# Kernel tuning notes

Hardware: AMD Instinct MI355X
Metric: run time of the kernel (lower is better)

The kernel has to match this reference:

```python
import jax, jax.numpy as jnp
import numpy as np

B, V, C, H, W, D = 1, 3, 32, 320, 320, 32


def setup_inputs() -> dict:
    key = jax.random.key(0)
    ks = jax.random.split(key, 14)
    feats = jax.random.normal(ks[0], (B, V, C, H, W), jnp.float32)
    # Valid pinhole projections: P = [[K @ [R|t]], [0,0,0,1]], identity rotation,
    # horizontal baselines sized so the warp stays mostly in-image over the depth range.
    K = np.array([[400.0, 0.0, W / 2.0], [0.0, 400.0, H / 2.0], [0.0, 0.0, 1.0]])
    mats = []
    for tx in (0.0, 100.0, -100.0):
        Rt = np.eye(4)
        Rt[0, 3] = tx
        P = np.eye(4)
        P[:3, :4] = K @ Rt[:3, :4]
        mats.append(P)
    proj = jnp.asarray(np.broadcast_to(np.stack(mats)[None], (B, V, 4, 4)).copy(), jnp.float32)
    planes = jnp.linspace(425.0, 935.0, D, dtype=jnp.float32)
    depth_values = jnp.broadcast_to(planes[None, :, None, None], (B, D, H, W)).astype(jnp.float32)
    s = 0.05  # small init so exp(reg_cost) stays well-scaled
    W0 = s * jax.random.normal(ks[1], (8, C, 3, 3), jnp.float32)
    Ws1 = s * jax.random.normal(ks[2], (8, 8, 3, 3), jnp.float32)
    W1 = s * jax.random.normal(ks[3], (16, 8, 3, 3), jnp.float32)
    Ws2 = s * jax.random.normal(ks[4], (16, 16, 3, 3), jnp.float32)
    W2 = s * jax.random.normal(ks[5], (32, 16, 3, 3), jnp.float32)
    Ws3 = s * jax.random.normal(ks[6], (32, 32, 3, 3), jnp.float32)
    W3 = s * jax.random.normal(ks[7], (64, 32, 3, 3), jnp.float32)
    Ws4 = s * jax.random.normal(ks[8], (64, 64, 3, 3), jnp.float32)
    U4 = s * jax.random.normal(ks[9], (32, 64, 1, 1), jnp.float32)
    U3 = s * jax.random.normal(ks[10], (16, 32, 1, 1), jnp.float32)
    U2 = s * jax.random.normal(ks[11], (8, 16, 1, 1), jnp.float32)
    Wout = s * jax.random.normal(ks[12], (1, 8, 3, 3), jnp.float32)
    return dict(feats=feats, proj=proj, depth_values=depth_values, W0=W0, Ws1=Ws1,
                W1=W1, Ws2=Ws2, W2=W2, Ws3=Ws3, W3=W3, Ws4=Ws4, U4=U4, U3=U3, U2=U2, Wout=Wout)


def _conv(x, w, stride=1):
    return jax.lax.conv_general_dilated(x, w, (stride, stride), 'SAME',
                                        dimension_numbers=('NCHW', 'OIHW', 'NCHW'))


def _up2(x):
    return jnp.repeat(jnp.repeat(x, 2, axis=2), 2, axis=3)


def _bilinear(img, x, y):
    # img [C,H,W]; x,y [N] pixel coords; zero padding, align_corners semantics
    Cc, Hh, Ww = img.shape
    x0 = jnp.floor(x)
    y0 = jnp.floor(y)
    wx = x - x0
    wy = y - y0

    def tap(xi, yi):
        valid = ((xi >= 0) & (xi <= Ww - 1) & (yi >= 0) & (yi <= Hh - 1)).astype(img.dtype)
        xc = jnp.clip(xi, 0, Ww - 1).astype(jnp.int32)
        yc = jnp.clip(yi, 0, Hh - 1).astype(jnp.int32)
        return img[:, yc, xc] * valid  # [C,N]

    return (tap(x0, y0) * (1 - wx) * (1 - wy) + tap(x0 + 1, y0) * wx * (1 - wy)
            + tap(x0, y0 + 1) * (1 - wx) * wy + tap(x0 + 1, y0 + 1) * wx * wy)


def _forward(feats, proj, depth_values, W0, Ws1, W1, Ws2, W2, Ws3, W3, Ws4, U4, U3, U2, Wout):
    Bn, Vn, Cn, Hn, Wn = feats.shape
    Dn = depth_values.shape[1]
    N = Hn * Wn
    relu = jax.nn.relu
    ref = feats[:, 0]
    ref_sq = ref * ref
    # Precompute per-src-view rotated pixel rays and translations.
    inv_ref = jnp.linalg.inv(proj[:, 0])                       # [B,4,4]
    rel = jnp.einsum('bvij,bjk->bvik', proj[:, 1:], inv_ref)   # [B,V-1,4,4]
    rot, trans = rel[:, :, :3, :3], rel[:, :, :3, 3]
    ys, xs = jnp.meshgrid(jnp.arange(Hn), jnp.arange(Wn), indexing='ij')
    pix = jnp.stack([xs.ravel(), ys.ravel(), jnp.ones(N)], 0).astype(feats.dtype)  # [3,N]
    rot_pix = jnp.einsum('bvij,jn->bvin', rot, pix)            # [B,V-1,3,N]

    def regularize(x, s1, s2, s3, s4):
        c1 = relu(_conv(x, W0) + _conv(s1, Ws1))
        c2 = relu(_conv(c1, W1, 2) + _conv(s2, Ws2))
        c3 = relu(_conv(c2, W2, 2) + _conv(s3, Ws3))
        c4 = relu(_conv(c3, W3, 2) + _conv(s4, Ws4))
        u3 = c3 + _up2(_conv(c4, U4))
        u2 = c2 + _up2(_conv(u3, U3))
        u1 = c1 + _up2(_conv(u2, U2))
        return _conv(u1, Wout), c1, c2, c3, c4

    def step(carry, depth_slice):  # depth_slice [B,H,W]
        s1, s2, s3, s4, exp_sum, depth_img, max_prob = carry
        vol_sum, vol_sq = ref, ref_sq
        dflat = depth_slice.reshape(Bn, 1, N)
        for v in range(Vn - 1):
            xyz = rot_pix[:, v] * dflat + trans[:, v, :, None]   # [B,3,N]
            px = xyz[:, 0] / xyz[:, 2]
            py = xyz[:, 1] / xyz[:, 2]
            warped = jax.vmap(_bilinear)(feats[:, v + 1], px, py).reshape(Bn, Cn, Hn, Wn)
            vol_sum = vol_sum + warped
            vol_sq = vol_sq + warped * warped
        variance = vol_sq / Vn - (vol_sum / Vn) ** 2
        cost, s1, s2, s3, s4 = regularize(variance, s1, s2, s3, s4)
        prob = jnp.exp(cost)                                     # [B,1,H,W]
        max_prob = jnp.maximum(max_prob, prob)                   # == flag*prob + (1-flag)*max
        depth_img = depth_img + depth_slice[:, None] * prob
        exp_sum = exp_sum + prob
        return (s1, s2, s3, s4, exp_sum, depth_img, max_prob), None

    z = lambda c, h, w: jnp.zeros((Bn, c, h, w), feats.dtype)
    init = (z(8, Hn, Wn), z(16, Hn // 2, Wn // 2), z(32, Hn // 4, Wn // 4), z(64, Hn // 8, Wn // 8),
            z(1, Hn, Wn), z(1, Hn, Wn), z(1, Hn, Wn))
    carry, _ = jax.lax.scan(step, init, jnp.moveaxis(depth_values, 1, 0))
    _, _, _, _, exp_sum, depth_img, max_prob = carry
    es = exp_sum + 1e-10
    depth_map = (depth_img / es)[:, 0]
    prob_map = (max_prob / es)[:, 0]
    return jnp.stack([depth_map, prob_map], axis=1)  # [B,2,H,W]


def reference(feats, proj, depth_values, W0, Ws1, W1, Ws2, W2, Ws3, W3, Ws4, U4, U3, U2, Wout):
    return _forward(feats, proj, depth_values, W0, Ws1, W1, Ws2, W2, Ws3, W3, Ws4, U4, U3, U2, Wout)
```

## Files before the change

kernel.cpp:

```cpp
#include <hip/hip_runtime.h>
#include <hip/hip_fp16.h>
#include <math.h>

#define HH 320
#define WW 320
#define NP (HH*WW)
#define CC 32
#define DD 32

#define H2 160
#define W2 160
#define N2 (H2*W2)
#define H4 80
#define W4 80
#define N4 (H4*W4)
#define H8 40
#define W8 40
#define N8 (H8*W8)

#define HALO 18
#define NHALO (HALO*HALO)

#define C1SZ (8*NP)
#define C2SZ (16*N2)
#define C3SZ (32*N4)
#define C4SZ (64*N8)

#define SMEM_FLOATS 5344

#define OFF_REL   0
#define OFF_C1R   64
#define OFF_C2R   (OFF_C1R + 5*C1SZ)
#define OFF_C3R   (OFF_C2R + 4*C2SZ)
#define OFF_C4R   (OFF_C3R + 3*C3SZ)
#define OFF_ESUM  (OFF_C4R + 2*C4SZ)
#define OFF_DIMG  (OFF_ESUM + NP)
#define OFF_MAXP  (OFF_DIMG + NP)
#define OFF_ACCE  (OFF_MAXP + NP)
#define OFF_FT    OFF_ACCE
#define OFF_END   (OFF_FT + (3*CC*NP)/2)

__global__ void k_prep(const float* __restrict__ proj, float* __restrict__ rel) {
    if (threadIdx.x != 0 || blockIdx.x != 0) return;
    float a[4][4], inv[4][4];
#pragma unroll
    for (int i = 0; i < 4; i++)
#pragma unroll
        for (int j = 0; j < 4; j++) {
            a[i][j] = proj[i*4 + j];
            inv[i][j] = (i == j) ? 1.0f : 0.0f;
        }
#pragma unroll
    for (int c = 0; c < 4; c++) {
        float s = 1.0f / a[c][c];
#pragma unroll
        for (int j = 0; j < 4; j++) { a[c][j] *= s; inv[c][j] *= s; }
#pragma unroll
        for (int r = 0; r < 4; r++) if (r != c) {
            float f = a[r][c];
#pragma unroll
            for (int j = 0; j < 4; j++) {
                a[r][j] -= f * a[c][j];
                inv[r][j] -= f * inv[c][j];
            }
        }
    }
#pragma unroll
    for (int v = 1; v < 3; v++) {
        const float* P = proj + v*16;
        float rm[3][4];
#pragma unroll
        for (int i = 0; i < 3; i++)
#pragma unroll
            for (int j = 0; j < 4; j++) {
                float s = 0.0f;
#pragma unroll
                for (int k = 0; k < 4; k++) s += P[i*4 + k] * inv[k][j];
                rm[i][j] = s;
            }
        float* o = rel + (v-1)*12;
        o[0]=rm[0][0]; o[1]=rm[0][1]; o[2]=rm[0][2];
        o[3]=rm[1][0]; o[4]=rm[1][1]; o[5]=rm[1][2];
        o[6]=rm[2][0]; o[7]=rm[2][1]; o[8]=rm[2][2];
        o[9]=rm[0][3]; o[10]=rm[1][3]; o[11]=rm[2][3];
    }
}

__global__ __launch_bounds__(256) void k_transpose(const float* __restrict__ feats,
                                                   __half* __restrict__ featsT) {
    __shared__ float lds[32][65];
    int g = blockIdx.x;
    int v = g / 1600;
    int p0 = (g - v*1600) * 64;
    const float* src = feats + (size_t)v*CC*NP + p0;
    for (int i = threadIdx.x; i < 32*64; i += 256) {
        int c = i >> 6, pp = i & 63;
        lds[c][pp] = src[(size_t)c*NP + pp];
    }
    __syncthreads();
    __half* dst = featsT + ((size_t)v*NP + p0)*32;
    int pp = threadIdx.x >> 2, cq = (threadIdx.x & 3) * 8;
    __half2 h[4];
#pragma unroll
    for (int j = 0; j < 4; j++)
        h[j] = __floats2half2_rn(lds[cq+2*j][pp], lds[cq+2*j+1][pp]);
    *(float4*)(dst + (size_t)pp*32 + cq) = *(float4*)h;
}

__device__ __forceinline__ void set_hline16(const __half* base, float* s) {
    const float4* q = (const float4*)base;
#pragma unroll
    for (int i = 0; i < 2; i++) {
        float4 raw = q[i];
        const __half2* h2 = (const __half2*)&raw;
#pragma unroll
        for (int j = 0; j < 4; j++) {
            float2 f = __half22float2(h2[j]);
            s[i*8 + 2*j]     = f.x;
            s[i*8 + 2*j + 1] = f.y;
        }
    }
}
__device__ __forceinline__ void acc_hline16(const __half* base, float w, float* t) {
    const float4* q = (const float4*)base;
#pragma unroll
    for (int i = 0; i < 2; i++) {
        float4 raw = q[i];
        const __half2* h2 = (const __half2*)&raw;
#pragma unroll
        for (int j = 0; j < 4; j++) {
            float2 f = __half22float2(h2[j]);
            t[i*8 + 2*j]     += f.x * w;
            t[i*8 + 2*j + 1] += f.y * w;
        }
    }
}

__device__ __forceinline__ int band_tile(int blk) { return (blk & 7) * 50 + (blk >> 3); }


__device__ void stageA(int blk, int d, int useT,
        const float* __restrict__ feats, const __half* __restrict__ featsT,
        const float* __restrict__ rel,
        const float* __restrict__ depthv, const float* __restrict__ c1r,
        const float* __restrict__ W0, const float* __restrict__ Ws1,
        float* smem) {
    __half2* pbuf = (__half2*)smem;
    float* fbuf = smem;
    const float* dslice = depthv + (size_t)d * NP;
    const float* s1 = c1r + (size_t)((d+4)%5) * C1SZ;
    float* c1out = (float*)c1r + (size_t)(d%5) * C1SZ;

    int L = band_tile(blk);
    int bx = L % 20, by = L / 20;
    int ox0 = bx*16, oy0 = by*16;

    const float inv3 = 1.0f / 3.0f;

    int opx = threadIdx.x & 15, opy = threadIdx.x >> 4;
    int obase = opy*HALO + opx;
    int outp = (oy0 + opy)*WW + ox0 + opx;

#pragma unroll 1
    for (int s = 0; s < 2; s++) {
        int hp = threadIdx.x + s*256;
        if (hp >= NHALO) break;
        int hy = hp / HALO, hx = hp - hy*HALO;
        int gy = oy0 + hy - 1, gx = ox0 + hx - 1;
        if (gy < 0 || gy >= HH || gx < 0 || gx >= WW) {
            __half2 z = __floats2half2_rn(0.0f, 0.0f);
#pragma unroll 1
            for (int c = 0; c < 16; c++) pbuf[c*NHALO + hp] = z;
            continue;
        }
        int p = gy*WW + gx;
        float depth = dslice[p];
        float fx = (float)gx, fy = (float)gy;

        int offs[8]; float wts[8];
#pragma unroll 1
        for (int v = 0; v < 2; v++) {
            const float* r = rel + v*12;
            float X = (r[0]*fx + r[1]*fy + r[2]) * depth + r[9];
            float Y = (r[3]*fx + r[4]*fy + r[5]) * depth + r[10];
            float Z = (r[6]*fx + r[7]*fy + r[8]) * depth + r[11];
            float iz = 1.0f / Z;
            float px = X * iz, py = Y * iz;
            float x0f = floorf(px), y0f = floorf(py);
            float wx = px - x0f, wy = py - y0f;
            int x0 = (int)x0f, y0 = (int)y0f;
#pragma unroll
            for (int t = 0; t < 4; t++) {
                int xi = x0 + (t & 1), yi = y0 + (t >> 1);
                float wgt = ((t & 1) ? wx : 1.0f - wx) * ((t >> 1) ? wy : 1.0f - wy);
                bool valid = (xi >= 0) && (xi <= WW-1) && (yi >= 0) && (yi <= HH-1);
                int xc = min(max(xi, 0), WW-1);
                int yc = min(max(yi, 0), HH-1);
                offs[v*4 + t] = yc*WW + xc;
                wts[v*4 + t] = valid ? wgt : 0.0f;
            }
        }

#pragma unroll 1
        for (int half = 0; half < 2; half++) {
            int cb = half * 16;
            float sum[16], sq[16], t[16];
            if (useT) {
                set_hline16(featsT + ((size_t)p << 5) + cb, sum);
#pragma unroll
                for (int c = 0; c < 16; c++) sq[c] = sum[c]*sum[c];
#pragma unroll 1
                for (int v = 0; v < 2; v++) {
                    const __half* fv = featsT + (size_t)(v+1)*CC*NP;
#pragma unroll
                    for (int c = 0; c < 16; c++) t[c] = 0.0f;
#pragma unroll 1
                    for (int tp = 0; tp < 4; tp++)
                        acc_hline16(fv + ((size_t)offs[v*4+tp] << 5) + cb,
                                    wts[v*4+tp], t);
#pragma unroll
                    for (int c = 0; c < 16; c++) { sum[c] += t[c]; sq[c] += t[c]*t[c]; }
                }
            } else {
                const float* f1 = feats + CC*NP;
                const float* f2 = feats + 2*CC*NP;
#pragma unroll 1
                for (int c = 0; c < 16; c++) {
                    int cg = cb + c;
                    float rv = feats[cg*NP + p];
                    const float* b1 = f1 + cg*NP;
                    float t1 = b1[offs[0]]*wts[0] + b1[offs[1]]*wts[1]
                             + b1[offs[2]]*wts[2] + b1[offs[3]]*wts[3];
                    const float* b2 = f2 + cg*NP;
                    float t2 = b2[offs[4]]*wts[4] + b2[offs[5]]*wts[5]
                             + b2[offs[6]]*wts[6] + b2[offs[7]]*wts[7];
                    sum[c] = rv + t1 + t2;
                    sq[c]  = rv*rv + t1*t1 + t2*t2;
                }
            }
#pragma unroll
            for (int c = 0; c < 8; c++) {
                float m0 = sum[2*c] * inv3,   v0 = sq[2*c] * inv3 - m0*m0;
                float m1 = sum[2*c+1] * inv3, v1 = sq[2*c+1] * inv3 - m1*m1;
                pbuf[(half*8 + c)*NHALO + hp] = __floats2half2_rn(v0, v1);
            }
        }
    }
    __syncthreads();

    float acc[8];
#pragma unroll
    for (int o = 0; o < 8; o++) acc[o] = 0.0f;

#pragma unroll 1
    for (int cp = 0; cp < 16; cp++) {
        float t0[9], t1[9];
#pragma unroll
        for (int ky = 0; ky < 3; ky++)
#pragma unroll
            for (int kx = 0; kx < 3; kx++) {
                __half2 h = pbuf[cp*NHALO + obase + ky*HALO + kx];
                t0[ky*3+kx] = __low2float(h);
                t1[ky*3+kx] = __high2float(h);
            }
#pragma unroll
        for (int o = 0; o < 8; o++) {
            const float* w0 = W0 + (o*32 + 2*cp)*9;
            float a = acc[o];
#pragma unroll
            for (int k = 0; k < 9; k++) a += t0[k] * w0[k];
#pragma unroll
            for (int k = 0; k < 9; k++) a += t1[k] * w0[9 + k];
            acc[o] = a;
        }
    }
    __syncthreads();

#pragma unroll 1
    for (int hp = threadIdx.x; hp < NHALO; hp += 256) {
        int hy = hp / HALO, hx = hp - hy*HALO;
        int gy = oy0 + hy - 1, gx = ox0 + hx - 1;
        bool v = (gy >= 0) && (gy < HH) && (gx >= 0) && (gx < WW);
        int p = v ? gy*WW + gx : 0;
#pragma unroll
        for (int c = 0; c < 8; c++) fbuf[c*NHALO + hp] = v ? s1[c*NP + p] : 0.0f;
    }
    __syncthreads();
#pragma unroll 1
    for (int ci = 0; ci < 8; ci++) {
        float t[9];
#pragma unroll
        for (int ky = 0; ky < 3; ky++)
#pragma unroll
            for (int kx = 0; kx < 3; kx++) t[ky*3+kx] = fbuf[ci*NHALO + obase + ky*HALO + kx];
#pragma unroll
        for (int o = 0; o < 8; o++) {
            const float* w = Ws1 + (o*8 + ci)*9;
            float a = acc[o];
#pragma unroll
            for (int k = 0; k < 9; k++) a += t[k] * w[k];
            acc[o] = a;
        }
    }
#pragma unroll
    for (int o = 0; o < 8; o++) c1out[o*NP + outp] = fmaxf(acc[o], 0.0f);
}

__device__ void stageB(int blk, int d,
        const float* __restrict__ c1r, const float* __restrict__ c2r_,
        const float* __restrict__ W1, const float* __restrict__ Ws2) {
    const float* c1 = c1r + (size_t)(d%5) * C1SZ;
    const float* s2 = c2r_ + (size_t)((d+3)%4) * C2SZ;
    float* c2 = (float*)c2r_ + (size_t)(d%4) * C2SZ;
    int p = (blk % 100)*256 + threadIdx.x;
    if (p >= N2) return;
    int og = blk / 100;
    int y = p / W2, x = p - y*W2;
    int offsA[9]; float mskA[9];
#pragma unroll
    for (int k = 0; k < 9; k++) {
        int yy = 2*y + k/3, xx = 2*x + k%3;
        bool v = (yy < HH) && (xx < WW);
        offsA[k] = v ? yy*WW + xx : 0;
        mskA[k] = v ? 1.0f : 0.0f;
    }
    int offsB[9]; float mskB[9];
#pragma unroll
    for (int k = 0; k < 9; k++) {
        int yy = y + k/3 - 1, xx = x + k%3 - 1;
        bool v = (yy >= 0) && (yy < H2) && (xx >= 0) && (xx < W2);
        offsB[k] = v ? yy*W2 + xx : 0;
        mskB[k] = v ? 1.0f : 0.0f;
    }
    float acc[8];
#pragma unroll
    for (int o = 0; o < 8; o++) acc[o] = 0.0f;
#pragma unroll 1
    for (int ci = 0; ci < 8; ci++) {
        const float* b = c1 + ci*NP;
        float t[9];
#pragma unroll
        for (int k = 0; k < 9; k++) t[k] = b[offsA[k]] * mskA[k];
#pragma unroll
        for (int o = 0; o < 8; o++) {
            const float* w = W1 + ((og*8 + o)*8 + ci)*9;
            float a = acc[o];
#pragma unroll
            for (int k = 0; k < 9; k++) a += t[k] * w[k];
            acc[o] = a;
        }
    }
#pragma unroll 1
    for (int ci = 0; ci < 16; ci++) {
        const float* b = s2 + ci*N2;
        float t[9];
#pragma unroll
        for (int k = 0; k < 9; k++) t[k] = b[offsB[k]] * mskB[k];
#pragma unroll
        for (int o = 0; o < 8; o++) {
            const float* w = Ws2 + ((og*8 + o)*16 + ci)*9;
            float a = acc[o];
#pragma unroll
            for (int k = 0; k < 9; k++) a += t[k] * w[k];
            acc[o] = a;
        }
    }
#pragma unroll
    for (int o = 0; o < 8; o++) c2[(og*8 + o)*N2 + p] = fmaxf(acc[o], 0.0f);
}

__device__ void stageC(int blk, int d,
        const float* __restrict__ c2r_, const float* __restrict__ c3r_,
        const float* __restrict__ W2w, const float* __restrict__ Ws3) {
    const float* c2 = c2r_ + (size_t)(d%4) * C2SZ;
    const float* s3 = c3r_ + (size_t)((d+2)%3) * C3SZ;
    float* c3 = (float*)c3r_ + (size_t)(d%3) * C3SZ;
    int p = (blk % 25)*256 + threadIdx.x;
    if (p >= N4) return;
    int og = blk / 25;
    int y = p / W4, x = p - y*W4;
    int offsA[9]; float mskA[9];
#pragma unroll
    for (int k = 0; k < 9; k++) {
        int yy = 2*y + k/3, xx = 2*x + k%3;
        bool v = (yy < H2) && (xx < W2);
        offsA[k] = v ? yy*W2 + xx : 0;
        mskA[k] = v ? 1.0f : 0.0f;
    }
    int offsB[9]; float mskB[9];
#pragma unroll
    for (int k = 0; k < 9; k++) {
        int yy = y + k/3 - 1, xx = x + k%3 - 1;
        bool v = (yy >= 0) && (yy < H4) && (xx >= 0) && (xx < W4);
        offsB[k] = v ? yy*W4 + xx : 0;
        mskB[k] = v ? 1.0f : 0.0f;
    }
    float acc[8];
#pragma unroll
    for (int o = 0; o < 8; o++) acc[o] = 0.0f;
#pragma unroll 1
    for (int ci = 0; ci < 16; ci++) {
        const float* b = c2 + ci*N2;
        float t[9];
#pragma unroll
        for (int k = 0; k < 9; k++) t[k] = b[offsA[k]] * mskA[k];
#pragma unroll
        for (int o = 0; o < 8; o++) {
            const float* w = W2w + ((og*8 + o)*16 + ci)*9;
            float a = acc[o];
#pragma unroll
            for (int k = 0; k < 9; k++) a += t[k] * w[k];
            acc[o] = a;
        }
    }
#pragma unroll 1
    for (int ci = 0; ci < 32; ci++) {
        const float* b = s3 + ci*N4;
        float t[9];
#pragma unroll
        for (int k = 0; k < 9; k++) t[k] = b[offsB[k]] * mskB[k];
#pragma unroll
        for (int o = 0; o < 8; o++) {
            const float* w = Ws3 + ((og*8 + o)*32 + ci)*9;
            float a = acc[o];
#pragma unroll
            for (int k = 0; k < 9; k++) a += t[k] * w[k];
            acc[o] = a;
        }
    }
#pragma unroll
    for (int o = 0; o < 8; o++) c3[(og*8 + o)*N4 + p] = fmaxf(acc[o], 0.0f);
}

__device__ void stageD(int blk, int d,
        const float* __restrict__ c3r_, const float* __restrict__ c4r_,
        const float* __restrict__ W3w, const float* __restrict__ Ws4) {
    const float* c3 = c3r_ + (size_t)(d%3) * C3SZ;
    const float* s4 = c4r_ + (size_t)((d+1)%2) * C4SZ;
    float* c4 = (float*)c4r_ + (size_t)(d%2) * C4SZ;
    int p = (blk % 7)*256 + threadIdx.x;
    if (p >= N8) return;
    int og = blk / 7;
    int y = p / W8, x = p - y*W8;
    int offsA[9]; float mskA[9];
#pragma unroll
    for (int k = 0; k < 9; k++) {
        int yy = 2*y + k/3, xx = 2*x + k%3;
        bool v = (yy < H4) && (xx < W4);
        offsA[k] = v ? yy*W4 + xx : 0;
        mskA[k] = v ? 1.0f : 0.0f;
    }
    int offsB[9]; float mskB[9];
#pragma unroll
    for (int k = 0; k < 9; k++) {
        int yy = y + k/3 - 1, xx = x + k%3 - 1;
        bool v = (yy >= 0) && (yy < H8) && (xx >= 0) && (xx < W8);
        offsB[k] = v ? yy*W8 + xx : 0;
        mskB[k] = v ? 1.0f : 0.0f;
    }
    float acc[8];
#pragma unroll
    for (int o = 0; o < 8; o++) acc[o] = 0.0f;
#pragma unroll 1
    for (int ci = 0; ci < 32; ci++) {
        const float* b = c3 + ci*N4;
        float t[9];
#pragma unroll
        for (int k = 0; k < 9; k++) t[k] = b[offsA[k]] * mskA[k];
#pragma unroll
        for (int o = 0; o < 8; o++) {
            const float* w = W3w + ((og*8 + o)*32 + ci)*9;
            float a = acc[o];
#pragma unroll
            for (int k = 0; k < 9; k++) a += t[k] * w[k];
            acc[o] = a;
        }
    }
#pragma unroll 1
    for (int ci = 0; ci < 64; ci++) {
        const float* b = s4 + ci*N8;
        float t[9];
#pragma unroll
        for (int k = 0; k < 9; k++) t[k] = b[offsB[k]] * mskB[k];
#pragma unroll
        for (int o = 0; o < 8; o++) {
            const float* w = Ws4 + ((og*8 + o)*64 + ci)*9;
            float a = acc[o];
#pragma unroll
            for (int k = 0; k < 9; k++) a += t[k] * w[k];
            acc[o] = a;
        }
    }
#pragma unroll
    for (int o = 0; o < 8; o++) c4[(og*8 + o)*N8 + p] = fmaxf(acc[o], 0.0f);
}

__device__ void stageU(int blk, int d,
        const float* __restrict__ c1r, const float* __restrict__ c2r_,
        const float* __restrict__ c3r_, const float* __restrict__ c4r_,
        const float* __restrict__ U4, const float* __restrict__ U3,
        const float* __restrict__ U2, const float* __restrict__ Wout,
        const float* __restrict__ depthv,
        float* __restrict__ exp_sum, float* __restrict__ depth_img,
        float* __restrict__ max_prob, float* smem) {
    const float* c1 = c1r + (size_t)(d%5) * C1SZ;
    const float* c2 = c2r_ + (size_t)(d%4) * C2SZ;
    const float* c3 = c3r_ + (size_t)(d%3) * C3SZ;
    const float* c4 = c4r_ + (size_t)(d%2) * C4SZ;
    const float* dslice = depthv + (size_t)d * NP;
    float* u3s = smem;
    float* u2s = smem + 32*36;
    float* u1s = smem + 32*36 + 16*100;

    int L = band_tile(blk);
    int bx = L % 20, by = L / 20;
    int ox0 = bx*16, oy0 = by*16;
    int qy0 = (oy0 >> 2) - 1, qx0 = (ox0 >> 2) - 1;
    int hy0 = (oy0 >> 1) - 1, hx0 = (ox0 >> 1) - 1;

#pragma unroll 1
    for (int i = threadIdx.x; i < 32*36; i += 256) {
        int ch = i / 36, pp = i - ch*36;
        int y4 = qy0 + pp/6, x4 = qx0 + pp%6;
        int y4c = min(max(y4, 0), H4-1), x4c = min(max(x4, 0), W4-1);
        int pl = (y4c >> 1)*W8 + (x4c >> 1);
        const float* w = U4 + ch*64;
        float s = c3[ch*N4 + y4c*W4 + x4c];
#pragma unroll 8
        for (int ci = 0; ci < 64; ci++) s += c4[ci*N8 + pl] * w[ci];
        u3s[ch*36 + pp] = s;
    }
    __syncthreads();
#pragma unroll 1
    for (int i = threadIdx.x; i < 16*100; i += 256) {
        int ch = i / 100, pp = i - ch*100;
        int y2 = hy0 + pp/10, x2 = hx0 + pp%10;
        int y2c = min(max(y2, 0), H2-1), x2c = min(max(x2, 0), W2-1);
        int ly = (y2c >> 1) - qy0, lx = (x2c >> 1) - qx0;
        const float* w = U3 + ch*32;
        float s = c2[ch*N2 + y2c*W2 + x2c];
#pragma unroll 8
        for (int ci = 0; ci < 32; ci++) s += u3s[ci*36 + ly*6 + lx] * w[ci];
        u2s[ch*100 + pp] = s;
    }
    __syncthreads();
#pragma unroll 1
    for (int i = threadIdx.x; i < 8*NHALO; i += 256) {
        int ch = i / NHALO, pp = i - ch*NHALO;
        int gy = oy0 + pp/HALO - 1, gx = ox0 + pp%HALO - 1;
        float s = 0.0f;
        if (gy >= 0 && gy < HH && gx >= 0 && gx < WW) {
            int ly = (gy >> 1) - hy0, lx = (gx >> 1) - hx0;
            const float* w = U2 + ch*16;
            s = c1[ch*NP + gy*WW + gx];
#pragma unroll
            for (int ci = 0; ci < 16; ci++) s += u2s[ci*100 + ly*10 + lx] * w[ci];
        }
        u1s[ch*NHALO + pp] = s;
    }
    __syncthreads();
    int px = threadIdx.x & 15, py = threadIdx.x >> 4;
    int base = py*HALO + px;
    float cost = 0.0f;
#pragma unroll 1
    for (int ci = 0; ci < 8; ci++) {
        const float* w = Wout + ci*9;
#pragma unroll
        for (int ky = 0; ky < 3; ky++)
#pragma unroll
            for (int kx = 0; kx < 3; kx++)
                cost += u1s[ci*NHALO + base + ky*HALO + kx] * w[ky*3 + kx];
    }
    int p = (oy0 + py)*WW + ox0 + px;
    float prob = expf(cost);
    exp_sum[p] += prob;
    depth_img[p] += dslice[p] * prob;
    max_prob[p] = fmaxf(max_prob[p], prob);
}

__global__ __launch_bounds__(256, 5) void k_uber(
        int t, int useT,
        const float* __restrict__ feats, const __half* __restrict__ featsT,
        const float* __restrict__ rel,
        const float* __restrict__ depthv,
        const float* __restrict__ W0, const float* __restrict__ Ws1,
        const float* __restrict__ W1, const float* __restrict__ Ws2,
        const float* __restrict__ W2w, const float* __restrict__ Ws3,
        const float* __restrict__ W3w, const float* __restrict__ Ws4,
        const float* __restrict__ U4, const float* __restrict__ U3,
        const float* __restrict__ U2, const float* __restrict__ Wout,
        float* __restrict__ c1r, float* __restrict__ c2r,
        float* __restrict__ c3r, float* __restrict__ c4r,
        float* __restrict__ esum, float* __restrict__ dimg,
        float* __restrict__ maxp) {
    __shared__ float smem[SMEM_FLOATS];
    int b = blockIdx.x;
    if (b < 400) {
        int d = t;
        if (d < DD) stageA(b, d, useT, feats, featsT, rel, depthv, c1r, W0, Ws1, smem);
    } else if (b < 600) {
        int d = t - 1;
        if (d >= 0 && d < DD) stageB(b - 400, d, c1r, c2r, W1, Ws2);
    } else if (b < 700) {
        int d = t - 2;
        if (d >= 0 && d < DD) stageC(b - 600, d, c2r, c3r, W2w, Ws3);
    } else if (b < 756) {
        int d = t - 3;
        if (d >= 0 && d < DD) stageD(b - 700, d, c3r, c4r, W3w, Ws4);
    } else {
        int d = t - 4;
        if (d >= 0 && d < DD)
            stageU(b - 756, d, c1r, c2r, c3r, c4r, U4, U3, U2, Wout, depthv,
                   esum, dimg, maxp, smem);
    }
}

__global__ __launch_bounds__(256) void k_final(
        const float* __restrict__ exp_sum, const float* __restrict__ depth_img,
        const float* __restrict__ max_prob, float* __restrict__ out) {
    int p = blockIdx.x*256 + threadIdx.x;
    if (p >= NP) return;
    float es = exp_sum[p] + 1e-10f;
    out[p] = depth_img[p] / es;
    out[NP + p] = max_prob[p] / es;
}

extern "C" void kernel_launch(void* const* d_in, const int* in_sizes, int n_in,
                              void* d_out, int out_size, void* d_ws, size_t ws_size,
                              hipStream_t stream) {
    const float* feats = (const float*)d_in[0];
    const float* proj  = (const float*)d_in[1];
    const float* depthv= (const float*)d_in[2];
    const float* W0  = (const float*)d_in[3];
    const float* Ws1 = (const float*)d_in[4];
    const float* W1  = (const float*)d_in[5];
    const float* Ws2 = (const float*)d_in[6];
    const float* W2w = (const float*)d_in[7];
    const float* Ws3 = (const float*)d_in[8];
    const float* W3w = (const float*)d_in[9];
    const float* Ws4 = (const float*)d_in[10];
    const float* U4  = (const float*)d_in[11];
    const float* U3  = (const float*)d_in[12];
    const float* U2  = (const float*)d_in[13];
    const float* Wout= (const float*)d_in[14];

    float* ws = (float*)d_ws;
    float* rel  = ws + OFF_REL;
    float* c1r  = ws + OFF_C1R;
    float* c2r  = ws + OFF_C2R;
    float* c3r  = ws + OFF_C3R;
    float* c4r  = ws + OFF_C4R;
    float* esum = ws + OFF_ESUM;
    float* dimg = ws + OFF_DIMG;
    float* maxp = ws + OFF_MAXP;

    int useT = (ws_size >= (size_t)OFF_END * sizeof(float)) ? 1 : 0;
    __half* featsT = (__half*)(useT ? (ws + OFF_FT) : ws);

    hipMemsetAsync(c1r, 0, (size_t)(OFF_ACCE - OFF_C1R) * sizeof(float), stream);
    k_prep<<<1, 1, 0, stream>>>(proj, rel);
    if (useT)
        k_transpose<<<dim3(3*1600), 256, 0, stream>>>(feats, featsT);

    for (int t = 0; t < DD + 4; t++) {
        k_uber<<<dim3(1156), 256, 0, stream>>>(t, useT, feats, featsT, rel, depthv,
            W0, Ws1, W1, Ws2, W2w, Ws3, W3w, Ws4, U4, U3, U2, Wout,
            c1r, c2r, c3r, c4r, esum, dimg, maxp);
    }
    k_final<<<dim3(400), 256, 0, stream>>>(esum, dimg, maxp, (float*)d_out);
}
```

Before: 2.839 ms.

## Fit uber-kernel into 1024 blocks with some blocks running two stage units

Shrinks the per-depth pipelined kernel grid from 1156 to 1024 blocks so it fills exactly four blocks per CU. Stage work is reordered: stage A and the upsample/output stage go first, then B. Blocks 800–931 also run a second unit covering the remaining stage C and D work. Launch bounds drop from 5 to 4 blocks per SM, giving the compiler more registers, and redundant bounds checks are removed because the pixel counts divide exactly by 256. The risk is that blocks doing two units serialize work and lengthen each step's critical path.

```diff
diff --git a/kernel.cpp b/kernel.cpp
--- a/kernel.cpp
+++ b/kernel.cpp
@@ -39,6 +39,8 @@
 #define OFF_ACCE  (OFF_MAXP + NP)
 #define OFF_FT    OFF_ACCE
 #define OFF_END   (OFF_FT + (3*CC*NP)/2)
+
+#define GRID 1024
 
 __global__ void k_prep(const float* __restrict__ proj, float* __restrict__ rel) {
     if (threadIdx.x != 0 || blockIdx.x != 0) return;
@@ -313,7 +315,6 @@
     const float* s2 = c2r_ + (size_t)((d+3)%4) * C2SZ;
     float* c2 = (float*)c2r_ + (size_t)(d%4) * C2SZ;
     int p = (blk % 100)*256 + threadIdx.x;
-    if (p >= N2) return;
     int og = blk / 100;
     int y = p / W2, x = p - y*W2;
     int offsA[9]; float mskA[9];
@@ -376,7 +377,6 @@
     const float* s3 = c3r_ + (size_t)((d+2)%3) * C3SZ;
     float* c3 = (float*)c3r_ + (size_t)(d%3) * C3SZ;
     int p = (blk % 25)*256 + threadIdx.x;
-    if (p >= N4) return;
     int og = blk / 25;
     int y = p / W4, x = p - y*W4;
     int offsA[9]; float mskA[9];
@@ -578,7 +578,35 @@
     max_prob[p] = fmaxf(max_prob[p], prob);
 }
 
-__global__ __launch_bounds__(256, 5) void k_uber(
+__device__ __forceinline__ void do_unit(int u, int t, int useT,
+        const float* feats, const __half* featsT, const float* rel,
+        const float* depthv,
+        const float* W0, const float* Ws1, const float* W1, const float* Ws2,
+        const float* W2w, const float* Ws3, const float* W3w, const float* Ws4,
+        const float* U4, const float* U3, const float* U2, const float* Wout,
+        float* c1r, float* c2r, float* c3r, float* c4r,
+        float* esum, float* dimg, float* maxp, float* smem) {
+    if (u < 400) {
+        int d = t;
+        if (d < DD) stageA(u, d, useT, feats, featsT, rel, depthv, c1r, W0, Ws1, smem);
+    } else if (u < 800) {
+        int d = t - 4;
+        if (d >= 0 && d < DD)
+            stageU(u - 400, d, c1r, c2r, c3r, c4r, U4, U3, U2, Wout, depthv,
+                   esum, dimg, maxp, smem);
+    } else if (u < 1000) {
+        int d = t - 1;
+        if (d >= 0 && d < DD) stageB(u - 800, d, c1r, c2r, W1, Ws2);
+    } else if (u < 1100) {
+        int d = t - 2;
+        if (d >= 0 && d < DD) stageC(u - 1000, d, c2r, c3r, W2w, Ws3);
+    } else {
+        int d = t - 3;
+        if (d >= 0 && d < DD) stageD(u - 1100, d, c3r, c4r, W3w, Ws4);
+    }
+}
+
+__global__ __launch_bounds__(256, 4) void k_uber(
         int t, int useT,
         const float* __restrict__ feats, const __half* __restrict__ featsT,
         const float* __restrict__ rel,
@@ -595,24 +623,13 @@
         float* __restrict__ maxp) {
     __shared__ float smem[SMEM_FLOATS];
     int b = blockIdx.x;
-    if (b < 400) {
-        int d = t;
-        if (d < DD) stageA(b, d, useT, feats, featsT, rel, depthv, c1r, W0, Ws1, smem);
-    } else if (b < 600) {
-        int d = t - 1;
-        if (d >= 0 && d < DD) stageB(b - 400, d, c1r, c2r, W1, Ws2);
-    } else if (b < 700) {
-        int d = t - 2;
-        if (d >= 0 && d < DD) stageC(b - 600, d, c2r, c3r, W2w, Ws3);
-    } else if (b < 756) {
-        int d = t - 3;
-        if (d >= 0 && d < DD) stageD(b - 700, d, c3r, c4r, W3w, Ws4);
-    } else {
-        int d = t - 4;
-        if (d >= 0 && d < DD)
-            stageU(b - 756, d, c1r, c2r, c3r, c4r, U4, U3, U2, Wout, depthv,
-                   esum, dimg, maxp, smem);
-    }
+    do_unit(b, t, useT, feats, featsT, rel, depthv, W0, Ws1, W1, Ws2,
+            W2w, Ws3, W3w, Ws4, U4, U3, U2, Wout,
+            c1r, c2r, c3r, c4r, esum, dimg, maxp, smem);
+    if (b >= 800 && b < 932)
+        do_unit(b + 224, t, useT, feats, featsT, rel, depthv, W0, Ws1, W1, Ws2,
+                W2w, Ws3, W3w, Ws4, U4, U3, U2, Wout,
+                c1r, c2r, c3r, c4r, esum, dimg, maxp, smem);
 }
 
 __global__ __launch_bounds__(256) void k_final(
@@ -663,7 +680,7 @@
         k_transpose<<<dim3(3*1600), 256, 0, stream>>>(feats, featsT);
 
     for (int t = 0; t < DD + 4; t++) {
-        k_uber<<<dim3(1156), 256, 0, stream>>>(t, useT, feats, featsT, rel, depthv,
+        k_uber<<<dim3(GRID), 256, 0, stream>>>(t, useT, feats, featsT, rel, depthv,
             W0, Ws1, W1, Ws2, W2w, Ws3, W3w, Ws4, U4, U3, U2, Wout,
             c1r, c2r, c3r, c4r, esum, dimg, maxp);
     }
```

Result: slower. 3.087 ms (+8.8%).
